# Optimization experiments

Hardware: AMD Instinct MI355X
Metric: run time of the kernel (lower is better)

Reference implementation:

```python
import jax, jax.numpy as jnp
import numpy as np

H = 16      # num_heads
HD = 128    # head_dim
P = 5       # num_paths
STAT = 4
HIDDEN = 2048
GATE_IN = HIDDEN + H * STAT * P + H * P + H * (P * (P - 1) // 2)  # 2608
GATE_HID = HIDDEN // 2  # 1024
OUT_DIM = H * P


def setup_inputs() -> dict:
    key = jax.random.key(0)
    ks = jax.random.split(key, 10)
    B, L = 2, 4096
    inp = {"hidden_states": jax.random.normal(ks[0], (B, L, HIDDEN), jnp.float32)}
    for i in range(P):
        inp[f"p{i}"] = jax.random.normal(ks[1 + i], (B, L, H, HD), jnp.float32)
    # QuantizedLinear treated as standard Linear (torch default init)
    s1 = 1.0 / np.sqrt(GATE_IN)
    s2 = 1.0 / np.sqrt(GATE_HID)
    inp["W1"] = jax.random.uniform(ks[6], (GATE_HID, GATE_IN), jnp.float32, -s1, s1)
    inp["b1"] = jax.random.uniform(ks[7], (GATE_HID,), jnp.float32, -s1, s1)
    inp["W2"] = jax.random.uniform(ks[8], (OUT_DIM, GATE_HID), jnp.float32, -s2, s2)
    # bias init: zero then favor paths 3 (value) and 4 (identity)
    b2 = np.zeros((H, P), np.float32)
    b2[:, 3] = 1.0
    b2[:, 4] = 2.0
    inp["b2"] = jnp.asarray(b2.reshape(-1))
    inp["log_temp"] = jnp.zeros((H, 1), jnp.float32)  # log(temp_init=1.0)
    return inp


def _forward(hidden_states, paths, W1, b1, W2, b2, log_temp):
    B, L, _ = hidden_states.shape
    ps = jnp.stack(paths, axis=-1)  # [B,L,H,D,P]
    # --- per-path stats over head_dim ---
    mean = ps.mean(axis=-2)                      # [B,L,H,P]
    var = ps.var(axis=-2)                        # unbiased=False
    abs_mean = jnp.abs(ps).mean(axis=-2)
    sq = jnp.sum(ps * ps, axis=-2)               # [B,L,H,P]
    l2 = jnp.sqrt(sq)
    stats = jnp.stack([mean, var, abs_mean, l2], axis=-1)   # [B,L,H,P,STAT] -> (p s) order
    stats_flat = stats.reshape(B, L, H, P * STAT)
    norms_flat = l2                                         # [B,L,H,P]
    # --- pairwise L2 distances: ||a-b||^2 = ||a||^2+||b||^2-2<a,b> ---
    dots = jnp.einsum('blhdp,blhdq->blhpq', ps, ps)
    d2 = sq[..., :, None] + sq[..., None, :] - 2.0 * dots
    dist = jnp.sqrt(jnp.clip(d2, 0.0, None))                # [B,L,H,P,P]
    iu0, iu1 = np.triu_indices(P, k=1)
    pairwise = dist[..., iu0, iu1]                           # [B,L,H,P*(P-1)/2]
    # --- router MLP ---
    gate_input = jnp.concatenate([
        hidden_states,
        stats_flat.reshape(B, L, -1),
        norms_flat.reshape(B, L, -1),
        pairwise.reshape(B, L, -1),
    ], axis=-1)  # [B,L,GATE_IN]
    h = jax.nn.gelu(gate_input @ W1.T + b1, approximate=False)
    logits = (h @ W2.T + b2).reshape(B, L, H, P)
    temp = jnp.exp(log_temp)[None, None]                     # [1,1,H,1]
    probs = jax.nn.softmax(logits / temp, axis=-1)
    probs = jnp.clip(probs, 0.02, None)
    probs = probs / probs.sum(axis=-1, keepdims=True)
    output = jnp.einsum('blhdp,blhp->blhd', ps, probs)       # [B,L,H,HD]
    return output


def reference(hidden_states, p0, p1, p2, p3, p4, W1, b1, W2, b2, log_temp):
    out = _forward(hidden_states, [p0, p1, p2, p3, p4], W1, b1, W2, b2, log_temp)
    reg_loss = jnp.float32(0.0)  # eval mode: no entropy regularizer
    return out, reg_loss
```

## Files before the change

### kernel.cpp

```cpp
#include <hip/hip_runtime.h>
#include <hip/hip_bf16.h>
#include <cstdint>
#include <cstddef>

typedef _Float16 half8 __attribute__((ext_vector_type(8)));
typedef float floatx4 __attribute__((ext_vector_type(4)));

#define KIN   2608
#define KP    2624
#define GH    1024
#define NOUT  80
#define NTOK  8192
#define HID   2048

__device__ __forceinline__ void async_copy16(const void* gsrc, void* ldst) {
  __builtin_amdgcn_global_load_lds(
      (const __attribute__((address_space(1))) void*)gsrc,
      (__attribute__((address_space(3))) void*)ldst, 16, 0, 0);
}

__device__ __forceinline__ float rsum16(float v) {
  v += __shfl_xor(v, 8, 16);
  v += __shfl_xor(v, 4, 16);
  v += __shfl_xor(v, 2, 16);
  v += __shfl_xor(v, 1, 16);
  return v;
}

__global__ __launch_bounds__(256) void convertw(
    const float* __restrict__ W1, const float* __restrict__ W2,
    _Float16* __restrict__ W1p, _Float16* __restrict__ W2p)
{
  int i = blockIdx.x * 256 + threadIdx.x;
  const int total1 = GH * KP;
  if (i < total1) {
    int n = i / KP;
    int k = i - n * KP;
    W1p[i] = (k < KIN) ? (_Float16)W1[(size_t)n * KIN + k] : (_Float16)0.f;
  } else {
    int j = i - total1;
    if (j < NOUT * GH) W2p[j] = (_Float16)W2[j];
  }
}

__global__ __launch_bounds__(256) void k1_stats(
    const float* __restrict__ hidden,
    const float* __restrict__ p0, const float* __restrict__ p1,
    const float* __restrict__ p2, const float* __restrict__ p3,
    const float* __restrict__ p4,
    _Float16* __restrict__ gate)
{
  const int token = blockIdx.x;
  const int tid = threadIdx.x;
  const int h = tid >> 4;
  const int j = tid & 15;
  const float* paths[5] = {p0, p1, p2, p3, p4};
  float v[5][8];
  const size_t pbase = ((size_t)token * 16 + h) * 128 + (size_t)j * 8;
#pragma unroll
  for (int p = 0; p < 5; ++p) {
    const float4* q = (const float4*)(paths[p] + pbase);
    float4 x0 = q[0], x1 = q[1];
    v[p][0] = x0.x; v[p][1] = x0.y; v[p][2] = x0.z; v[p][3] = x0.w;
    v[p][4] = x1.x; v[p][5] = x1.y; v[p][6] = x1.z; v[p][7] = x1.w;
  }
  float s[5], s2[5], sa[5], dt[10];
#pragma unroll
  for (int p = 0; p < 5; ++p) {
    float a = 0.f, b = 0.f, c = 0.f;
#pragma unroll
    for (int e = 0; e < 8; ++e) { float x = v[p][e]; a += x; b += x * x; c += fabsf(x); }
    s[p] = a; s2[p] = b; sa[p] = c;
  }
  {
    int pi = 0;
#pragma unroll
    for (int a = 0; a < 5; ++a)
#pragma unroll
      for (int b = a + 1; b < 5; ++b) {
        float d = 0.f;
#pragma unroll
        for (int e = 0; e < 8; ++e) d += v[a][e] * v[b][e];
        dt[pi++] = d;
      }
  }
#pragma unroll
  for (int p = 0; p < 5; ++p) { s[p] = rsum16(s[p]); s2[p] = rsum16(s2[p]); sa[p] = rsum16(sa[p]); }
#pragma unroll
  for (int i = 0; i < 10; ++i) dt[i] = rsum16(dt[i]);

  _Float16* gs = gate + (size_t)token * KP;
  if (j == 0) {
#pragma unroll
    for (int p = 0; p < 5; ++p) {
      float mean = s[p] * (1.f / 128.f);
      float var  = s2[p] * (1.f / 128.f) - mean * mean;
      float am   = sa[p] * (1.f / 128.f);
      float l2   = sqrtf(s2[p]);
      gs[2048 + h * 20 + p * 4 + 0] = (_Float16)mean;
      gs[2048 + h * 20 + p * 4 + 1] = (_Float16)var;
      gs[2048 + h * 20 + p * 4 + 2] = (_Float16)am;
      gs[2048 + h * 20 + p * 4 + 3] = (_Float16)l2;
      gs[2368 + h * 5 + p] = (_Float16)l2;
    }
    int pi = 0;
#pragma unroll
    for (int a = 0; a < 5; ++a)
#pragma unroll
      for (int b = a + 1; b < 5; ++b) {
        float d2 = s2[a] + s2[b] - 2.f * dt[pi];
        gs[2448 + h * 10 + pi] = (_Float16)sqrtf(fmaxf(d2, 0.f));
        ++pi;
      }
  }
  {
    const float4* hs = (const float4*)(hidden + (size_t)token * HID);
    float4 a = hs[tid * 2], b = hs[tid * 2 + 1];
    half8 hv;
    hv[0] = (_Float16)a.x; hv[1] = (_Float16)a.y; hv[2] = (_Float16)a.z; hv[3] = (_Float16)a.w;
    hv[4] = (_Float16)b.x; hv[5] = (_Float16)b.y; hv[6] = (_Float16)b.z; hv[7] = (_Float16)b.w;
    *(half8*)(gs + tid * 8) = hv;
  }
  if (tid == 0) {
#pragma unroll
    for (int i = KIN; i < KP; ++i) gs[i] = (_Float16)0.f;
  }
}

__global__ __launch_bounds__(256) void gemm1(
    const _Float16* __restrict__ A,
    const _Float16* __restrict__ Bt,
    const float* __restrict__ b1,
    _Float16* __restrict__ Hm)
{
  __shared__ _Float16 As[128 * 64];
  __shared__ _Float16 Bs[128 * 64];
  const int tid  = threadIdx.x;
  const int lane = tid & 63;
  const int wave = tid >> 6;
  const int m0 = blockIdx.x * 128;
  const int n0 = blockIdx.y * 128;
  const int wm = (wave & 1) * 64;
  const int wn = (wave >> 1) * 64;

  floatx4 acc[4][4];
#pragma unroll
  for (int i = 0; i < 4; ++i)
#pragma unroll
    for (int k = 0; k < 4; ++k) acc[i][k] = (floatx4){0.f, 0.f, 0.f, 0.f};

  for (int kt = 0; kt < KP / 64; ++kt) {
    __syncthreads();
    const int kbase = kt * 64;
#pragma unroll
    for (int r = 0; r < 4; ++r) {
      int chunk = r * 256 + tid;
      int row = chunk >> 3;
      int kk  = (chunk & 7) * 8;
      const _Float16* ga = A  + (size_t)(m0 + row) * KP + kbase + kk;
      const _Float16* gb = Bt + (size_t)(n0 + row) * KP + kbase + kk;
      async_copy16(ga, &As[0] + (r * 2048 + wave * 512));
      async_copy16(gb, &Bs[0] + (r * 2048 + wave * 512));
    }
    __syncthreads();
#pragma unroll
    for (int ks = 0; ks < 2; ++ks) {
      half8 af[4], bf[4];
#pragma unroll
      for (int i = 0; i < 4; ++i) {
        int ar = wm + i * 16 + (lane & 15);
        af[i] = *(const half8*)&As[ar * 64 + ks * 32 + (lane >> 4) * 8];
        int br = wn + i * 16 + (lane & 15);
        bf[i] = *(const half8*)&Bs[br * 64 + ks * 32 + (lane >> 4) * 8];
      }
#pragma unroll
      for (int mi = 0; mi < 4; ++mi)
#pragma unroll
        for (int ni = 0; ni < 4; ++ni)
          acc[mi][ni] = __builtin_amdgcn_mfma_f32_16x16x32_f16(af[mi], bf[ni], acc[mi][ni], 0, 0, 0);
    }
  }
#pragma unroll
  for (int mi = 0; mi < 4; ++mi) {
#pragma unroll
    for (int ni = 0; ni < 4; ++ni) {
      int col = n0 + wn + ni * 16 + (lane & 15);
      float bias = b1[col];
#pragma unroll
      for (int r = 0; r < 4; ++r) {
        int row = m0 + wm + mi * 16 + (lane >> 4) * 4 + r;
        float x = acc[mi][ni][r] + bias;
        float g = 0.5f * x * (1.f + erff(x * 0.70710678118654752f));
        Hm[(size_t)row * GH + col] = (_Float16)g;
      }
    }
  }
}

__global__ __launch_bounds__(256) void gemm2(
    const _Float16* __restrict__ Hm, const _Float16* __restrict__ W2p,
    const float* __restrict__ b2, float* __restrict__ logits)
{
  const int lane = threadIdx.x & 63;
  const int wave = threadIdx.x >> 6;
  const int m0 = blockIdx.x * 64 + wave * 16;
  const int mrow = m0 + (lane & 15);
  const int koff = (lane >> 4) * 8;
  floatx4 acc[5];
#pragma unroll
  for (int i = 0; i < 5; ++i) acc[i] = (floatx4){0.f, 0.f, 0.f, 0.f};
  for (int k0 = 0; k0 < GH; k0 += 32) {
    half8 af = *(const half8*)&Hm[(size_t)mrow * GH + k0 + koff];
#pragma unroll
    for (int ni = 0; ni < 5; ++ni) {
      half8 bf = *(const half8*)&W2p[(size_t)(ni * 16 + (lane & 15)) * GH + k0 + koff];
      acc[ni] = __builtin_amdgcn_mfma_f32_16x16x32_f16(af, bf, acc[ni], 0, 0, 0);
    }
  }
#pragma unroll
  for (int ni = 0; ni < 5; ++ni) {
    int col = ni * 16 + (lane & 15);
    float bias = b2[col];
#pragma unroll
    for (int r = 0; r < 4; ++r) {
      int row = m0 + (lane >> 4) * 4 + r;
      logits[(size_t)row * NOUT + col] = acc[ni][r] + bias;
    }
  }
}

__global__ __launch_bounds__(256) void softmaxk(
    const float* __restrict__ logits, const float* __restrict__ log_temp,
    float* __restrict__ probs)
{
  int id = blockIdx.x * 256 + threadIdx.x;
  int t = id >> 4;
  int h = id & 15;
  float it = __expf(-log_temp[h]);
  const float* lp = logits + (size_t)t * NOUT + h * 5;
  float x[5];
  float m = -1e30f;
#pragma unroll
  for (int p = 0; p < 5; ++p) { x[p] = lp[p] * it; m = fmaxf(m, x[p]); }
  float ssum = 0.f;
#pragma unroll
  for (int p = 0; p < 5; ++p) { x[p] = __expf(x[p] - m); ssum += x[p]; }
  float inv = 1.f / ssum;
  float c = 0.f;
#pragma unroll
  for (int p = 0; p < 5; ++p) { x[p] = fmaxf(x[p] * inv, 0.02f); c += x[p]; }
  float inv2 = 1.f / c;
  float* pp = probs + (size_t)t * NOUT + h * 5;
#pragma unroll
  for (int p = 0; p < 5; ++p) pp[p] = x[p] * inv2;
}

__global__ __launch_bounds__(256) void k5_combine(
    const float* __restrict__ p0, const float* __restrict__ p1,
    const float* __restrict__ p2, const float* __restrict__ p3,
    const float* __restrict__ p4,
    const float* __restrict__ probs, float* __restrict__ out)
{
  size_t i4 = (size_t)blockIdx.x * 256 + threadIdx.x;
  int token = (int)(i4 >> 9);
  int rem = (int)(i4 & 511);
  int h = rem >> 5;
  const float* pb = probs + (size_t)token * NOUT + h * 5;
  float w0 = pb[0], w1 = pb[1], w2 = pb[2], w3 = pb[3], w4 = pb[4];
  size_t off = i4 * 4;
  float4 a0 = *(const float4*)(p0 + off);
  float4 a1 = *(const float4*)(p1 + off);
  float4 a2 = *(const float4*)(p2 + off);
  float4 a3 = *(const float4*)(p3 + off);
  float4 a4 = *(const float4*)(p4 + off);
  float4 r;
  r.x = a0.x * w0 + a1.x * w1 + a2.x * w2 + a3.x * w3 + a4.x * w4;
  r.y = a0.y * w0 + a1.y * w1 + a2.y * w2 + a3.y * w3 + a4.y * w4;
  r.z = a0.z * w0 + a1.z * w1 + a2.z * w2 + a3.z * w3 + a4.z * w4;
  r.w = a0.w * w0 + a1.w * w1 + a2.w * w2 + a3.w * w3 + a4.w * w4;
  *(float4*)(out + off) = r;
  if (i4 == 0) out[(size_t)NTOK * 2048] = 0.f;
}

extern "C" void kernel_launch(void* const* d_in, const int* in_sizes, int n_in,
                              void* d_out, int out_size, void* d_ws, size_t ws_size,
                              hipStream_t stream) {
  const float* hidden  = (const float*)d_in[0];
  const float* p0      = (const float*)d_in[1];
  const float* p1      = (const float*)d_in[2];
  const float* p2      = (const float*)d_in[3];
  const float* p3      = (const float*)d_in[4];
  const float* p4      = (const float*)d_in[5];
  const float* W1      = (const float*)d_in[6];
  const float* b1      = (const float*)d_in[7];
  const float* W2      = (const float*)d_in[8];
  const float* b2      = (const float*)d_in[9];
  const float* logtemp = (const float*)d_in[10];
  float* out = (float*)d_out;

  char* ws = (char*)d_ws;
  _Float16* gate = (_Float16*)(ws);
  _Float16* W1p  = (_Float16*)(ws + 42991616);
  _Float16* W2p  = (_Float16*)(ws + 48365568);
  _Float16* Hm   = (_Float16*)(ws + 48529408);
  float*    logits = (float*)(ws + 65306624);
  float*    probs  = (float*)(ws + 67928064);

  convertw<<<10816, 256, 0, stream>>>(W1, W2, W1p, W2p);
  k1_stats<<<NTOK, 256, 0, stream>>>(hidden, p0, p1, p2, p3, p4, gate);
  gemm1<<<dim3(NTOK / 128, GH / 128), 256, 0, stream>>>(gate, W1p, b1, Hm);
  gemm2<<<NTOK / 64, 256, 0, stream>>>(Hm, W2p, b2, logits);
  softmaxk<<<(NTOK * 16) / 256, 256, 0, stream>>>(logits, logtemp, probs);
  k5_combine<<<(NTOK * 2048 / 4) / 256, 256, 0, stream>>>(p0, p1, p2, p3, p4, probs, out);
}
```

Before: 565.1 us.

## Compute path stats with one thread per token-head and split hidden conversion

Reassigns the path-statistics kernel so each thread handles a full token-head, accumulating sums and pairwise dots serially and removing the cross-lane shuffle reductions. The hidden-state fp16 conversion moves into its own kernel, and the stats writes become vectorized. This removes shuffle overhead and redundant per-lane work, but it cuts thread-level parallelism and makes loads strided across lanes, which may hurt memory coalescing.

```diff
diff --git a/kernel.cpp b/kernel.cpp
--- a/kernel.cpp
+++ b/kernel.cpp
@@ -4,6 +4,8 @@
 #include <cstddef>
 
 typedef _Float16 half8 __attribute__((ext_vector_type(8)));
+typedef _Float16 half4 __attribute__((ext_vector_type(4)));
+typedef _Float16 half2v __attribute__((ext_vector_type(2)));
 typedef float floatx4 __attribute__((ext_vector_type(4)));
 
 #define KIN   2608
@@ -17,14 +19,6 @@
   __builtin_amdgcn_global_load_lds(
       (const __attribute__((address_space(1))) void*)gsrc,
       (__attribute__((address_space(3))) void*)ldst, 16, 0, 0);
-}
-
-__device__ __forceinline__ float rsum16(float v) {
-  v += __shfl_xor(v, 8, 16);
-  v += __shfl_xor(v, 4, 16);
-  v += __shfl_xor(v, 2, 16);
-  v += __shfl_xor(v, 1, 16);
-  return v;
 }
 
 __global__ __launch_bounds__(256) void convertw(
@@ -43,36 +37,56 @@
   }
 }
 
+__global__ __launch_bounds__(256) void convh(
+    const float* __restrict__ hidden, _Float16* __restrict__ gate)
+{
+  int i = blockIdx.x * 256 + threadIdx.x;
+  int token = i >> 8;
+  int c = i & 255;
+  const float4* src = (const float4*)(hidden + (size_t)token * HID + c * 8);
+  float4 a = src[0], b = src[1];
+  half8 hv;
+  hv[0] = (_Float16)a.x; hv[1] = (_Float16)a.y; hv[2] = (_Float16)a.z; hv[3] = (_Float16)a.w;
+  hv[4] = (_Float16)b.x; hv[5] = (_Float16)b.y; hv[6] = (_Float16)b.z; hv[7] = (_Float16)b.w;
+  *(half8*)(gate + (size_t)token * KP + c * 8) = hv;
+}
+
 __global__ __launch_bounds__(256) void k1_stats(
-    const float* __restrict__ hidden,
     const float* __restrict__ p0, const float* __restrict__ p1,
     const float* __restrict__ p2, const float* __restrict__ p3,
     const float* __restrict__ p4,
     _Float16* __restrict__ gate)
 {
-  const int token = blockIdx.x;
-  const int tid = threadIdx.x;
-  const int h = tid >> 4;
-  const int j = tid & 15;
+  const int gid = blockIdx.x * 256 + threadIdx.x;
+  const int token = gid >> 4;
+  const int h = gid & 15;
+  const size_t base = (size_t)gid * 128;
   const float* paths[5] = {p0, p1, p2, p3, p4};
-  float v[5][8];
-  const size_t pbase = ((size_t)token * 16 + h) * 128 + (size_t)j * 8;
-#pragma unroll
-  for (int p = 0; p < 5; ++p) {
-    const float4* q = (const float4*)(paths[p] + pbase);
-    float4 x0 = q[0], x1 = q[1];
-    v[p][0] = x0.x; v[p][1] = x0.y; v[p][2] = x0.z; v[p][3] = x0.w;
-    v[p][4] = x1.x; v[p][5] = x1.y; v[p][6] = x1.z; v[p][7] = x1.w;
-  }
+
   float s[5], s2[5], sa[5], dt[10];
 #pragma unroll
-  for (int p = 0; p < 5; ++p) {
-    float a = 0.f, b = 0.f, c = 0.f;
-#pragma unroll
-    for (int e = 0; e < 8; ++e) { float x = v[p][e]; a += x; b += x * x; c += fabsf(x); }
-    s[p] = a; s2[p] = b; sa[p] = c;
-  }
-  {
+  for (int p = 0; p < 5; ++p) { s[p] = 0.f; s2[p] = 0.f; sa[p] = 0.f; }
+#pragma unroll
+  for (int i = 0; i < 10; ++i) dt[i] = 0.f;
+
+#pragma unroll 2
+  for (int c = 0; c < 16; ++c) {
+    float v[5][8];
+#pragma unroll
+    for (int p = 0; p < 5; ++p) {
+      const float4* q = (const float4*)(paths[p] + base + c * 8);
+      float4 x0 = q[0], x1 = q[1];
+      v[p][0] = x0.x; v[p][1] = x0.y; v[p][2] = x0.z; v[p][3] = x0.w;
+      v[p][4] = x1.x; v[p][5] = x1.y; v[p][6] = x1.z; v[p][7] = x1.w;
+    }
+#pragma unroll
+    for (int p = 0; p < 5; ++p) {
+#pragma unroll
+      for (int e = 0; e < 8; ++e) {
+        float x = v[p][e];
+        s[p] += x; s2[p] += x * x; sa[p] += fabsf(x);
+      }
+    }
     int pi = 0;
 #pragma unroll
     for (int a = 0; a < 5; ++a)
@@ -81,49 +95,48 @@
         float d = 0.f;
 #pragma unroll
         for (int e = 0; e < 8; ++e) d += v[a][e] * v[b][e];
-        dt[pi++] = d;
-      }
-  }
-#pragma unroll
-  for (int p = 0; p < 5; ++p) { s[p] = rsum16(s[p]); s2[p] = rsum16(s2[p]); sa[p] = rsum16(sa[p]); }
-#pragma unroll
-  for (int i = 0; i < 10; ++i) dt[i] = rsum16(dt[i]);
+        dt[pi++] += d;
+      }
+  }
 
   _Float16* gs = gate + (size_t)token * KP;
-  if (j == 0) {
-#pragma unroll
-    for (int p = 0; p < 5; ++p) {
-      float mean = s[p] * (1.f / 128.f);
-      float var  = s2[p] * (1.f / 128.f) - mean * mean;
-      float am   = sa[p] * (1.f / 128.f);
-      float l2   = sqrtf(s2[p]);
-      gs[2048 + h * 20 + p * 4 + 0] = (_Float16)mean;
-      gs[2048 + h * 20 + p * 4 + 1] = (_Float16)var;
-      gs[2048 + h * 20 + p * 4 + 2] = (_Float16)am;
-      gs[2048 + h * 20 + p * 4 + 3] = (_Float16)l2;
-      gs[2368 + h * 5 + p] = (_Float16)l2;
-    }
+  float l2v[5];
+#pragma unroll
+  for (int p = 0; p < 5; ++p) {
+    float mean = s[p] * (1.f / 128.f);
+    float var  = s2[p] * (1.f / 128.f) - mean * mean;
+    float am   = sa[p] * (1.f / 128.f);
+    float l2   = sqrtf(s2[p]);
+    l2v[p] = l2;
+    half4 st;
+    st[0] = (_Float16)mean; st[1] = (_Float16)var;
+    st[2] = (_Float16)am;   st[3] = (_Float16)l2;
+    *(half4*)(gs + 2048 + h * 20 + p * 4) = st;
+  }
+#pragma unroll
+  for (int p = 0; p < 5; ++p) gs[2368 + h * 5 + p] = (_Float16)l2v[p];
+  {
+    float pw[10];
     int pi = 0;
 #pragma unroll
     for (int a = 0; a < 5; ++a)
 #pragma unroll
       for (int b = a + 1; b < 5; ++b) {
         float d2 = s2[a] + s2[b] - 2.f * dt[pi];
-        gs[2448 + h * 10 + pi] = (_Float16)sqrtf(fmaxf(d2, 0.f));
+        pw[pi] = sqrtf(fmaxf(d2, 0.f));
         ++pi;
       }
-  }
-  {
-    const float4* hs = (const float4*)(hidden + (size_t)token * HID);
-    float4 a = hs[tid * 2], b = hs[tid * 2 + 1];
-    half8 hv;
-    hv[0] = (_Float16)a.x; hv[1] = (_Float16)a.y; hv[2] = (_Float16)a.z; hv[3] = (_Float16)a.w;
-    hv[4] = (_Float16)b.x; hv[5] = (_Float16)b.y; hv[6] = (_Float16)b.z; hv[7] = (_Float16)b.w;
-    *(half8*)(gs + tid * 8) = hv;
-  }
-  if (tid == 0) {
-#pragma unroll
-    for (int i = KIN; i < KP; ++i) gs[i] = (_Float16)0.f;
+#pragma unroll
+    for (int i = 0; i < 5; ++i) {
+      half2v t; t[0] = (_Float16)pw[2 * i]; t[1] = (_Float16)pw[2 * i + 1];
+      *(half2v*)(gs + 2448 + h * 10 + 2 * i) = t;
+    }
+  }
+  if (h == 0) {
+    half8 z = {(_Float16)0.f, (_Float16)0.f, (_Float16)0.f, (_Float16)0.f,
+               (_Float16)0.f, (_Float16)0.f, (_Float16)0.f, (_Float16)0.f};
+    *(half8*)(gs + 2608) = z;
+    *(half8*)(gs + 2616) = z;
   }
 }
 
@@ -307,7 +320,8 @@
   float*    probs  = (float*)(ws + 67928064);
 
   convertw<<<10816, 256, 0, stream>>>(W1, W2, W1p, W2p);
-  k1_stats<<<NTOK, 256, 0, stream>>>(hidden, p0, p1, p2, p3, p4, gate);
+  convh<<<8192, 256, 0, stream>>>(hidden, gate);
+  k1_stats<<<512, 256, 0, stream>>>(p0, p1, p2, p3, p4, gate);
   gemm1<<<dim3(NTOK / 128, GH / 128), 256, 0, stream>>>(gate, W1p, b1, Hm);
   gemm2<<<NTOK / 64, 256, 0, stream>>>(Hm, W2p, b2, logits);
   softmaxk<<<(NTOK * 16) / 256, 256, 0, stream>>>(logits, logtemp, probs);
```

Result: slower. 607.6 us (+7.5%).
